# Kernel tuning notes

Measured on AMD Instinct MI355X. Metric: run time of the kernel, lower is better.

## Reference

```python
import jax, jax.numpy as jnp
import numpy as np


def _bd(x, W, b):
    # block-diagonal linear: x [B, D] -> [B, Dout], W [H, D/H, Dout/H], b [Dout]
    B, D = x.shape
    H = W.shape[0]
    y = jnp.einsum('bhi,hio->bho', x.reshape(B, H, D // H), W)
    return y.reshape(B, -1) + b


def setup_inputs() -> dict:
    key = jax.random.key(0)
    ks = jax.random.split(key, 16)
    B, D, H = 8192, 1024, 8
    U = int(D * 4 / 3)  # 1365
    d = D // H          # 128
    s = 0.05
    f32 = jnp.float32
    return {
        'x': jax.random.normal(ks[0], (B, D), f32),
        'h_prev': jax.random.normal(ks[1], (B, D), f32),
        'c_prev': jax.random.normal(ks[2], (B, D), f32),
        'n_prev': jax.random.uniform(ks[3], (B, D), f32) + 0.5,  # positive normalizer state
        'm_prev': jax.random.normal(ks[4], (B, D), f32),
        'ln_g': jnp.ones((D,), f32),
        'ln_b': jnp.zeros((D,), f32),
        'conv_w': jax.random.normal(ks[5], (1, 1, 4), f32) * 0.5,
        'conv_b': jax.random.normal(ks[6], (1,), f32) * 0.1,
        'W': jax.random.normal(ks[7], (4, H, d, d), f32) * s,   # gates z,i,f,o input projections
        'bW': jax.random.normal(ks[8], (4, D), f32) * s,
        'R': jax.random.normal(ks[9], (4, H, d, d), f32) * s,   # gates z,i,f,o recurrent projections
        'bR': jax.random.normal(ks[10], (4, D), f32) * s,
        'upl_w': jax.random.normal(ks[11], (D, U), f32) * s,
        'upl_b': jnp.zeros((U,), f32),
        'upr_w': jax.random.normal(ks[12], (D, U), f32) * s,
        'upr_b': jnp.zeros((U,), f32),
        'down_w': jax.random.normal(ks[13], (U, D), f32) * s,
        'down_b': jnp.zeros((D,), f32),
    }


def reference(x, h_prev, c_prev, n_prev, m_prev, ln_g, ln_b, conv_w, conv_b,
              W, bW, R, bR, upl_w, upl_b, upr_w, upr_b, down_w, down_b):
    # LayerNorm over feature dim (eps matches torch default 1e-5)
    mu = jnp.mean(x, axis=-1, keepdims=True)
    var = jnp.var(x, axis=-1, keepdims=True)
    x_norm = (x - mu) * jax.lax.rsqrt(var + 1e-5) * ln_g + ln_b
    # causal conv1d along the feature axis: kernel 4, left-pad 3 (Conv1d(1,1,4))
    conv = jax.lax.conv_general_dilated(
        x_norm[:, None, :], conv_w, window_strides=(1,), padding=[(3, 0)],
        dimension_numbers=('NCH', 'OIH', 'NCH'))[:, 0, :] + conv_b
    x_conv = jax.nn.silu(conv)
    # block-diagonal gate pre-activations (gate order in W/R stacks: z, i, f, o)
    z = jnp.tanh(_bd(x, W[0], bW[0]) + _bd(h_prev, R[0], bR[0]))
    o = jax.nn.sigmoid(_bd(x, W[3], bW[3]) + _bd(h_prev, R[3], bR[3]))
    i_tilde = _bd(x_conv, W[1], bW[1]) + _bd(h_prev, R[1], bR[1])
    f_tilde = _bd(x_conv, W[2], bW[2]) + _bd(h_prev, R[2], bR[2])
    # stabilized exp-max gating
    m_t = jnp.maximum(f_tilde + m_prev, i_tilde)
    i = jnp.exp(i_tilde - m_t)
    f = jnp.exp(f_tilde + m_prev - m_t)
    c_t = f * c_prev + i * z
    n_t = f * n_prev + i
    h_t = o * c_t / n_t
    # gated MLP (torch F.gelu default = exact erf gelu)
    left = h_t @ upl_w + upl_b
    right = jax.nn.gelu(h_t @ upr_w + upr_b, approximate=False)
    output = (left * right) @ down_w + down_b
    return (output, h_t, c_t, n_t, m_t)
```

## Files before the change

### kernel.cpp

```cpp
#include <hip/hip_runtime.h>
#include <hip/hip_bf16.h>

typedef __attribute__((ext_vector_type(8))) short s8v;
typedef __attribute__((ext_vector_type(4))) float f4v;
typedef unsigned short us4 __attribute__((ext_vector_type(4)));

#define NB 8192
#define ND 1024
#define NH 8
#define NU 1365
#define NUP 1408
#define GK 384
#define GN 512
static const size_t BD = (size_t)NB * ND;

#define WS_AG   ((size_t)0)
#define WS_G    ((size_t)50331648)
#define WS_HBF  ((size_t)73400320)
#define WS_WG   ((size_t)90177536)
#define WS_ULR  ((size_t)93323264)
#define WS_DWNT ((size_t)99090432)

__device__ __forceinline__ void gload16(const void* g, void* l) {
  __builtin_amdgcn_global_load_lds((const __attribute__((address_space(1))) void*)g,
                                   (__attribute__((address_space(3))) void*)l, 16, 0, 0);
}
__device__ __forceinline__ unsigned short tobf(float f) {
  unsigned int u = __float_as_uint(f);
  unsigned int r = (u + 0x7FFFu + ((u >> 16) & 1u)) >> 16;
  return (unsigned short)r;
}
__device__ __forceinline__ float frombf(unsigned short u) {
  return __uint_as_float(((unsigned int)u) << 16);
}
__device__ __forceinline__ float sigm(float x) { return 1.f / (1.f + expf(-x)); }
__device__ __forceinline__ f4v mfma16(s8v a, s8v b, f4v c) {
  return __builtin_amdgcn_mfma_f32_16x16x32_bf16(a, b, c, 0, 0, 0);
}

__global__ __launch_bounds__(256) void prep_kernel(
    const float* __restrict__ W, const float* __restrict__ R,
    const float* __restrict__ upl, const float* __restrict__ upr,
    const float* __restrict__ dwn,
    unsigned short* __restrict__ Wg, unsigned short* __restrict__ ULR,
    unsigned short* __restrict__ Dt) {
  long long idx = (long long)blockIdx.x * 256 + threadIdx.x;
  const long long N1 = (long long)4096 * GK;
  const long long N3 = (long long)2 * NUP * ND;
  const long long N2 = (long long)NUP * ND;
  if (idx < N1) {
    int c = (int)(idx / GK), k = (int)(idx % GK);
    int j = c & 15, g = (c >> 4) & 3, cgrp = (c >> 6) & 7, h = c >> 9;
    int o = cgrp * 16 + j;
    float v = 0.f;
    if (k < 128) {
      if (g == 0 || g == 3) v = W[(((size_t)g * NH + h) * 128 + k) * 128 + o];
    } else if (k < 256) {
      if (g == 1 || g == 2) v = W[(((size_t)g * NH + h) * 128 + (k - 128)) * 128 + o];
    } else {
      v = R[(((size_t)g * NH + h) * 128 + (k - 256)) * 128 + o];
    }
    Wg[idx] = tobf(v);
    return;
  }
  idx -= N1;
  if (idx < N3) {
    int r = (int)(idx / ND), k = (int)(idx % ND);
    int o = (r >> 4) & 1;
    int gcol = (r >> 5) * 16 + (r & 15);
    float v = 0.f;
    if (gcol < NU) v = o ? upr[(size_t)k * NU + gcol] : upl[(size_t)k * NU + gcol];
    ULR[idx] = tobf(v);
    return;
  }
  idx -= N3;
  if (idx < N2) { int n = (int)(idx / NUP), k = (int)(idx % NUP);
    Dt[idx] = (k < NU) ? tobf(dwn[(size_t)k * ND + n]) : 0; return; }
}

__global__ __launch_bounds__(256) void norm_conv(
    const float* __restrict__ x, const float* __restrict__ hp,
    const float* __restrict__ lg, const float* __restrict__ lb,
    const float* __restrict__ cw, const float* __restrict__ cb,
    unsigned short* __restrict__ Ag) {
  const int b = blockIdx.x, tid = threadIdx.x;
  const int lane = tid & 63, wv = tid >> 6;
  __shared__ float xs[1024];
  __shared__ float red[8];
  const int d0 = tid * 4;
  float4 xv = *(const float4*)(x + (size_t)b * ND + d0);
  float s = xv.x + xv.y + xv.z + xv.w;
  float ss = xv.x * xv.x + xv.y * xv.y + xv.z * xv.z + xv.w * xv.w;
#pragma unroll
  for (int o = 32; o; o >>= 1) { s += __shfl_down(s, o); ss += __shfl_down(ss, o); }
  if (lane == 0) { red[wv] = s; red[4 + wv] = ss; }
  __syncthreads();
  float S = red[0] + red[1] + red[2] + red[3];
  float SS = red[4] + red[5] + red[6] + red[7];
  float mu = S * (1.f / ND);
  float var = SS * (1.f / ND) - mu * mu;
  float rstd = rsqrtf(var + 1e-5f);
  float xn[4];
#pragma unroll
  for (int t = 0; t < 4; ++t) {
    float xx = (&xv.x)[t];
    xn[t] = (xx - mu) * rstd * lg[d0 + t] + lb[d0 + t];
    xs[d0 + t] = xn[t];
  }
  __syncthreads();
  float w0 = cw[0], w1 = cw[1], w2 = cw[2], w3 = cw[3], cbv = cb[0];
  float cv[4];
#pragma unroll
  for (int t = 0; t < 4; ++t) {
    int d = d0 + t;
    float a = cbv + w3 * xs[d];
    if (d >= 1) a += w2 * xs[d - 1];
    if (d >= 2) a += w1 * xs[d - 2];
    if (d >= 3) a += w0 * xs[d - 3];
    cv[t] = a * (1.f / (1.f + expf(-a)));
  }
  float4 hv = *(const float4*)(hp + (size_t)b * ND + d0);
  const int h = d0 >> 7, j = d0 & 127;
  us4 px, pc, ph;
#pragma unroll
  for (int t = 0; t < 4; ++t) { px[t] = tobf((&xv.x)[t]); pc[t] = tobf(cv[t]); ph[t] = tobf((&hv.x)[t]); }
  size_t base = (size_t)b * 3072 + (size_t)h * 384 + j;
  *(us4*)(Ag + base) = px;
  *(us4*)(Ag + base + 128) = pc;
  *(us4*)(Ag + base + 256) = ph;
}

__global__ __launch_bounds__(256) void gate_fused(
    const unsigned short* __restrict__ Ag, const unsigned short* __restrict__ Wg,
    const float* __restrict__ bW, const float* __restrict__ bR,
    const float* __restrict__ cp, const float* __restrict__ np_,
    const float* __restrict__ mp,
    float* __restrict__ dout, unsigned short* __restrict__ Hb) {
  __shared__ short As[2][128 * 32];
  __shared__ short Bs[2][128 * 32];
  const int tid = threadIdx.x, lane = tid & 63, wv = tid >> 6;
  const int wm = wv >> 1, wn = wv & 1;
  const int row0 = blockIdx.x * 128;
  const int p = blockIdx.y;
  const int h = blockIdx.z;
  const int srow = wv * 32 + (lane >> 2), scol = (lane & 3) * 8;
  const unsigned short* At = Ag + (size_t)h * 384;
  const unsigned short* Bt = Wg + ((size_t)h * 512 + (size_t)p * 128) * GK;
#define STG(bb, k0)                                                                     \
  do {                                                                                  \
    gload16(At + (size_t)(row0 + srow) * 3072 + (k0) + scol, (char*)As[bb] + wv * 2048);\
    gload16(At + (size_t)(row0 + srow + 16) * 3072 + (k0) + scol,                       \
            (char*)As[bb] + wv * 2048 + 1024);                                          \
    gload16(Bt + (size_t)srow * GK + (k0) + scol, (char*)Bs[bb] + wv * 2048);           \
    gload16(Bt + (size_t)(srow + 16) * GK + (k0) + scol,                                \
            (char*)Bs[bb] + wv * 2048 + 1024);                                          \
  } while (0)
  f4v acc[4][4] = {};
  STG(0, 0);
  __syncthreads();
  for (int kt = 0; kt < 12; ++kt) {
    const int cur = kt & 1;
    if (kt < 11) STG(cur ^ 1, (kt + 1) * 32);
    s8v a[4], b[4];
#pragma unroll
    for (int m = 0; m < 4; ++m)
      a[m] = *(const s8v*)&As[cur][(wm * 64 + m * 16 + (lane & 15)) * 32 + (lane >> 4) * 8];
#pragma unroll
    for (int g = 0; g < 4; ++g)
      b[g] = *(const s8v*)&Bs[cur][(wn * 64 + g * 16 + (lane & 15)) * 32 + (lane >> 4) * 8];
#pragma unroll
    for (int m = 0; m < 4; ++m)
#pragma unroll
      for (int g = 0; g < 4; ++g) acc[m][g] = mfma16(a[m], b[g], acc[m][g]);
    __syncthreads();
  }
#undef STG
  const int cgrp = p * 2 + wn;
  const int gcol = h * 128 + cgrp * 16 + (lane & 15);
  const float Bz = bW[gcol] + bR[gcol];
  const float Bi = bW[ND + gcol] + bR[ND + gcol];
  const float Bf = bW[2 * ND + gcol] + bR[2 * ND + gcol];
  const float Bo = bW[3 * ND + gcol] + bR[3 * ND + gcol];
#pragma unroll
  for (int m = 0; m < 4; ++m) {
    const int rbase = row0 + wm * 64 + m * 16 + (lane >> 4) * 4;
#pragma unroll
    for (int r = 0; r < 4; ++r) {
      const size_t idx = (size_t)(rbase + r) * ND + gcol;
      float zt = tanhf(acc[m][0][r] + Bz);
      float it = acc[m][1][r] + Bi;
      float ft = acc[m][2][r] + Bf;
      float ot = sigm(acc[m][3][r] + Bo);
      float mv = mp[idx];
      float mt = fmaxf(ft + mv, it);
      float ii = expf(it - mt);
      float ff = expf(ft + mv - mt);
      float ct = ff * cp[idx] + ii * zt;
      float nt = ff * np_[idx] + ii;
      float ht = ot * ct / nt;
      dout[BD + idx] = ht;
      dout[2 * BD + idx] = ct;
      dout[3 * BD + idx] = nt;
      dout[4 * BD + idx] = mt;
      Hb[idx] = tobf(ht);
    }
  }
}

__global__ __launch_bounds__(256) void up_gemm(
    const unsigned short* __restrict__ A, const unsigned short* __restrict__ ULR,
    const float* __restrict__ lbias, const float* __restrict__ rbias,
    unsigned short* __restrict__ G) {
  __shared__ short As[2][4096];
  __shared__ short Bs[2][4096];
  const int tid = threadIdx.x, lane = tid & 63, wv = tid >> 6;
  const int wm = wv >> 1, wn = wv & 1;
  const int bid = blockIdx.x;
  const int swz = (bid & 7) * 176 + (bid >> 3);
  const int row0 = (swz / 22) * 128, n0 = (swz % 22) * 128;
  const int srow = wv * 32 + (lane >> 2), scol = (lane & 3) * 8;
#define STG(bb, k0)                                                                       \
  do {                                                                                    \
    gload16(A + (size_t)(row0 + srow) * 1024 + (k0) + scol, (char*)As[bb] + wv * 2048);   \
    gload16(A + (size_t)(row0 + srow + 16) * 1024 + (k0) + scol,                          \
            (char*)As[bb] + wv * 2048 + 1024);                                            \
    gload16(ULR + (size_t)(n0 + srow) * 1024 + (k0) + scol, (char*)Bs[bb] + wv * 2048);   \
    gload16(ULR + (size_t)(n0 + srow + 16) * 1024 + (k0) + scol,                          \
            (char*)Bs[bb] + wv * 2048 + 1024);                                            \
  } while (0)
  f4v acc[4][4] = {};
  STG(0, 0);
  __syncthreads();
  for (int kt = 0; kt < 32; ++kt) {
    const int cur = kt & 1;
    if (kt < 31) STG(cur ^ 1, (kt + 1) * 32);
    s8v a[4], b[4];
#pragma unroll
    for (int m = 0; m < 4; ++m)
      a[m] = *(const s8v*)&As[cur][(wm * 64 + m * 16 + (lane & 15)) * 32 + (lane >> 4) * 8];
#pragma unroll
    for (int n = 0; n < 4; ++n)
      b[n] = *(const s8v*)&Bs[cur][(wn * 64 + n * 16 + (lane & 15)) * 32 + (lane >> 4) * 8];
#pragma unroll
    for (int m = 0; m < 4; ++m)
#pragma unroll
      for (int n = 0; n < 4; ++n) acc[m][n] = mfma16(a[m], b[n], acc[m][n]);
    __syncthreads();
  }
#undef STG
  const int gb = (n0 >> 1) + wn * 32;
#pragma unroll
  for (int m = 0; m < 4; ++m) {
    const int row = row0 + wm * 64 + m * 16 + (lane >> 4) * 4;
#pragma unroll
    for (int p = 0; p < 2; ++p) {
      const int gcol = gb + p * 16 + (lane & 15);
      const bool ok = gcol < NU;
      const float bl_ = ok ? lbias[gcol] : 0.f;
      const float br_ = ok ? rbias[gcol] : 0.f;
#pragma unroll
      for (int r = 0; r < 4; ++r) {
        float L = acc[m][2 * p][r] + bl_;
        float Rv = acc[m][2 * p + 1][r] + br_;
        float ge = 0.5f * Rv * (1.f + erff(Rv * 0.70710678118654752f));
        G[(size_t)(row + r) * NUP + gcol] = ok ? tobf(L * ge) : (unsigned short)0;
      }
    }
  }
}

__global__ __launch_bounds__(256) void down_gemm(
    const unsigned short* __restrict__ A, const unsigned short* __restrict__ Bt,
    const float* __restrict__ dbias, float* __restrict__ out) {
  __shared__ short As[2][4096];
  __shared__ short Bs[2][4096];
  const int tid = threadIdx.x, lane = tid & 63, wv = tid >> 6;
  const int wm = wv >> 1, wn = wv & 1;
  const int bid = blockIdx.x;
  const int swz = (bid & 7) * 64 + (bid >> 3);
  const int row0 = (swz >> 3) * 128, n0 = (swz & 7) * 128;
  const int srow = wv * 32 + (lane >> 2), scol = (lane & 3) * 8;
#define STG(bb, k0)                                                                       \
  do {                                                                                    \
    gload16(A + (size_t)(row0 + srow) * NUP + (k0) + scol, (char*)As[bb] + wv * 2048);    \
    gload16(A + (size_t)(row0 + srow + 16) * NUP + (k0) + scol,                           \
            (char*)As[bb] + wv * 2048 + 1024);                                            \
    gload16(Bt + (size_t)(n0 + srow) * NUP + (k0) + scol, (char*)Bs[bb] + wv * 2048);     \
    gload16(Bt + (size_t)(n0 + srow + 16) * NUP + (k0) + scol,                            \
            (char*)Bs[bb] + wv * 2048 + 1024);                                            \
  } while (0)
  f4v acc[4][4] = {};
  STG(0, 0);
  __syncthreads();
  for (int kt = 0; kt < NUP / 32; ++kt) {
    const int cur = kt & 1;
    if (kt < NUP / 32 - 1) STG(cur ^ 1, (kt + 1) * 32);
    s8v a[4], b[4];
#pragma unroll
    for (int m = 0; m < 4; ++m)
      a[m] = *(const s8v*)&As[cur][(wm * 64 + m * 16 + (lane & 15)) * 32 + (lane >> 4) * 8];
#pragma unroll
    for (int n = 0; n < 4; ++n)
      b[n] = *(const s8v*)&Bs[cur][(wn * 64 + n * 16 + (lane & 15)) * 32 + (lane >> 4) * 8];
#pragma unroll
    for (int m = 0; m < 4; ++m)
#pragma unroll
      for (int n = 0; n < 4; ++n) acc[m][n] = mfma16(a[m], b[n], acc[m][n]);
    __syncthreads();
  }
#undef STG
#pragma unroll
  for (int m = 0; m < 4; ++m) {
    const int row = row0 + wm * 64 + m * 16 + (lane >> 4) * 4;
#pragma unroll
    for (int n = 0; n < 4; ++n) {
      const int col = n0 + wn * 64 + n * 16 + (lane & 15);
      const float bias = dbias[col];
#pragma unroll
      for (int r = 0; r < 4; ++r)
        out[(size_t)(row + r) * ND + col] = acc[m][n][r] + bias;
    }
  }
}

extern "C" void kernel_launch(void* const* d_in, const int* in_sizes, int n_in,
                              void* d_out, int out_size, void* d_ws, size_t ws_size,
                              hipStream_t stream) {
  const float* x    = (const float*)d_in[0];
  const float* hp   = (const float*)d_in[1];
  const float* cp   = (const float*)d_in[2];
  const float* np_  = (const float*)d_in[3];
  const float* mp   = (const float*)d_in[4];
  const float* lg   = (const float*)d_in[5];
  const float* lb   = (const float*)d_in[6];
  const float* cw   = (const float*)d_in[7];
  const float* cb   = (const float*)d_in[8];
  const float* W    = (const float*)d_in[9];
  const float* bW   = (const float*)d_in[10];
  const float* R    = (const float*)d_in[11];
  const float* bR   = (const float*)d_in[12];
  const float* upl  = (const float*)d_in[13];
  const float* uplb = (const float*)d_in[14];
  const float* upr  = (const float*)d_in[15];
  const float* uprb = (const float*)d_in[16];
  const float* dwn  = (const float*)d_in[17];
  const float* dwnb = (const float*)d_in[18];
  float* out = (float*)d_out;
  char* ws = (char*)d_ws;
  unsigned short* Ag  = (unsigned short*)(ws + WS_AG);
  unsigned short* G   = (unsigned short*)(ws + WS_G);
  unsigned short* Hb  = (unsigned short*)(ws + WS_HBF);
  unsigned short* Wg  = (unsigned short*)(ws + WS_WG);
  unsigned short* ULR = (unsigned short*)(ws + WS_ULR);
  unsigned short* Dt  = (unsigned short*)(ws + WS_DWNT);

  prep_kernel<<<23040, 256, 0, stream>>>(W, R, upl, upr, dwn, Wg, ULR, Dt);
  norm_conv<<<NB, 256, 0, stream>>>(x, hp, lg, lb, cw, cb, Ag);
  gate_fused<<<dim3(64, 4, 8), 256, 0, stream>>>(Ag, Wg, bW, bR, cp, np_, mp, out, Hb);
  up_gemm<<<1408, 256, 0, stream>>>(Hb, ULR, uplb, uprb, G);
  down_gemm<<<512, 256, 0, stream>>>(G, Dt, dwnb, out);
}
```

Measured before the change: 276.5 us.

## Drop LDS double buffering; gate GEMM loads fragments directly from global

The gate kernel becomes single-wavefront blocks of 64 rows by 64 gate columns that read MFMA operand fragments straight from global memory, with no LDS staging or barriers and a much larger grid. The up and down GEMMs change from double-buffered LDS staging to single-buffered load, sync, compute, sync loops, which halves LDS use and may raise occupancy. In exchange the GEMMs lose overlap between global loads and MFMA work, and the gate kernel gives up LDS reuse and issues strided uncoalesced global reads that depend on cache hits.

```diff
diff --git a/kernel.cpp b/kernel.cpp
--- a/kernel.cpp
+++ b/kernel.cpp
@@ -130,60 +130,44 @@
   *(us4*)(Ag + base + 256) = ph;
 }
 
-__global__ __launch_bounds__(256) void gate_fused(
+__global__ __launch_bounds__(64, 3) void gate_fused(
     const unsigned short* __restrict__ Ag, const unsigned short* __restrict__ Wg,
     const float* __restrict__ bW, const float* __restrict__ bR,
     const float* __restrict__ cp, const float* __restrict__ np_,
     const float* __restrict__ mp,
     float* __restrict__ dout, unsigned short* __restrict__ Hb) {
-  __shared__ short As[2][128 * 32];
-  __shared__ short Bs[2][128 * 32];
-  const int tid = threadIdx.x, lane = tid & 63, wv = tid >> 6;
-  const int wm = wv >> 1, wn = wv & 1;
-  const int row0 = blockIdx.x * 128;
-  const int p = blockIdx.y;
-  const int h = blockIdx.z;
-  const int srow = wv * 32 + (lane >> 2), scol = (lane & 3) * 8;
-  const unsigned short* At = Ag + (size_t)h * 384;
-  const unsigned short* Bt = Wg + ((size_t)h * 512 + (size_t)p * 128) * GK;
-#define STG(bb, k0)                                                                     \
-  do {                                                                                  \
-    gload16(At + (size_t)(row0 + srow) * 3072 + (k0) + scol, (char*)As[bb] + wv * 2048);\
-    gload16(At + (size_t)(row0 + srow + 16) * 3072 + (k0) + scol,                       \
-            (char*)As[bb] + wv * 2048 + 1024);                                          \
-    gload16(Bt + (size_t)srow * GK + (k0) + scol, (char*)Bs[bb] + wv * 2048);           \
-    gload16(Bt + (size_t)(srow + 16) * GK + (k0) + scol,                                \
-            (char*)Bs[bb] + wv * 2048 + 1024);                                          \
-  } while (0)
+  const int lane = threadIdx.x;
+  const int row0 = blockIdx.x * 64;
+  const int cg = blockIdx.y;
+  const int h = cg >> 3;
+  const unsigned short* Arow =
+      Ag + (size_t)(row0 + (lane & 15)) * 3072 + h * 384 + (lane >> 4) * 8;
+  const unsigned short* Brow =
+      Wg + (size_t)(cg * 64 + (lane & 15)) * GK + (lane >> 4) * 8;
   f4v acc[4][4] = {};
-  STG(0, 0);
-  __syncthreads();
+#pragma unroll
   for (int kt = 0; kt < 12; ++kt) {
-    const int cur = kt & 1;
-    if (kt < 11) STG(cur ^ 1, (kt + 1) * 32);
+    const int k0 = kt * 32;
     s8v a[4], b[4];
 #pragma unroll
     for (int m = 0; m < 4; ++m)
-      a[m] = *(const s8v*)&As[cur][(wm * 64 + m * 16 + (lane & 15)) * 32 + (lane >> 4) * 8];
+      a[m] = *(const s8v*)(Arow + (size_t)m * 16 * 3072 + k0);
 #pragma unroll
     for (int g = 0; g < 4; ++g)
-      b[g] = *(const s8v*)&Bs[cur][(wn * 64 + g * 16 + (lane & 15)) * 32 + (lane >> 4) * 8];
+      b[g] = *(const s8v*)(Brow + (size_t)g * 16 * GK + k0);
 #pragma unroll
     for (int m = 0; m < 4; ++m)
 #pragma unroll
       for (int g = 0; g < 4; ++g) acc[m][g] = mfma16(a[m], b[g], acc[m][g]);
-    __syncthreads();
-  }
-#undef STG
-  const int cgrp = p * 2 + wn;
-  const int gcol = h * 128 + cgrp * 16 + (lane & 15);
+  }
+  const int gcol = h * 128 + (cg & 7) * 16 + (lane & 15);
   const float Bz = bW[gcol] + bR[gcol];
   const float Bi = bW[ND + gcol] + bR[ND + gcol];
   const float Bf = bW[2 * ND + gcol] + bR[2 * ND + gcol];
   const float Bo = bW[3 * ND + gcol] + bR[3 * ND + gcol];
 #pragma unroll
   for (int m = 0; m < 4; ++m) {
-    const int rbase = row0 + wm * 64 + m * 16 + (lane >> 4) * 4;
+    const int rbase = row0 + m * 16 + (lane >> 4) * 4;
 #pragma unroll
     for (int r = 0; r < 4; ++r) {
       const size_t idx = (size_t)(rbase + r) * ND + gcol;
@@ -211,43 +195,33 @@
     const unsigned short* __restrict__ A, const unsigned short* __restrict__ ULR,
     const float* __restrict__ lbias, const float* __restrict__ rbias,
     unsigned short* __restrict__ G) {
-  __shared__ short As[2][4096];
-  __shared__ short Bs[2][4096];
+  __shared__ short As[4096];
+  __shared__ short Bs[4096];
   const int tid = threadIdx.x, lane = tid & 63, wv = tid >> 6;
   const int wm = wv >> 1, wn = wv & 1;
   const int bid = blockIdx.x;
   const int swz = (bid & 7) * 176 + (bid >> 3);
   const int row0 = (swz / 22) * 128, n0 = (swz % 22) * 128;
   const int srow = wv * 32 + (lane >> 2), scol = (lane & 3) * 8;
-#define STG(bb, k0)                                                                       \
-  do {                                                                                    \
-    gload16(A + (size_t)(row0 + srow) * 1024 + (k0) + scol, (char*)As[bb] + wv * 2048);   \
-    gload16(A + (size_t)(row0 + srow + 16) * 1024 + (k0) + scol,                          \
-            (char*)As[bb] + wv * 2048 + 1024);                                            \
-    gload16(ULR + (size_t)(n0 + srow) * 1024 + (k0) + scol, (char*)Bs[bb] + wv * 2048);   \
-    gload16(ULR + (size_t)(n0 + srow + 16) * 1024 + (k0) + scol,                          \
-            (char*)Bs[bb] + wv * 2048 + 1024);                                            \
-  } while (0)
   f4v acc[4][4] = {};
-  STG(0, 0);
-  __syncthreads();
   for (int kt = 0; kt < 32; ++kt) {
-    const int cur = kt & 1;
-    if (kt < 31) STG(cur ^ 1, (kt + 1) * 32);
+    const int k0 = kt * 32;
+    gload16(A + (size_t)(row0 + srow) * 1024 + k0 + scol, (char*)As + wv * 2048);
+    gload16(A + (size_t)(row0 + srow + 16) * 1024 + k0 + scol, (char*)As + wv * 2048 + 1024);
+    gload16(ULR + (size_t)(n0 + srow) * 1024 + k0 + scol, (char*)Bs + wv * 2048);
+    gload16(ULR + (size_t)(n0 + srow + 16) * 1024 + k0 + scol, (char*)Bs + wv * 2048 + 1024);
+    __syncthreads();
     s8v a[4], b[4];
 #pragma unroll
-    for (int m = 0; m < 4; ++m)
-      a[m] = *(const s8v*)&As[cur][(wm * 64 + m * 16 + (lane & 15)) * 32 + (lane >> 4) * 8];
-#pragma unroll
-    for (int n = 0; n < 4; ++n)
-      b[n] = *(const s8v*)&Bs[cur][(wn * 64 + n * 16 + (lane & 15)) * 32 + (lane >> 4) * 8];
+    for (int m = 0; m < 4; ++m) a[m] = *(const s8v*)&As[(wm * 64 + m * 16 + (lane & 15)) * 32 + (lane >> 4) * 8];
+#pragma unroll
+    for (int n = 0; n < 4; ++n) b[n] = *(const s8v*)&Bs[(wn * 64 + n * 16 + (lane & 15)) * 32 + (lane >> 4) * 8];
 #pragma unroll
     for (int m = 0; m < 4; ++m)
 #pragma unroll
       for (int n = 0; n < 4; ++n) acc[m][n] = mfma16(a[m], b[n], acc[m][n]);
     __syncthreads();
   }
-#undef STG
   const int gb = (n0 >> 1) + wn * 32;
 #pragma unroll
   for (int m = 0; m < 4; ++m) {
@@ -272,43 +246,33 @@
 __global__ __launch_bounds__(256) void down_gemm(
     const unsigned short* __restrict__ A, const unsigned short* __restrict__ Bt,
     const float* __restrict__ dbias, float* __restrict__ out) {
-  __shared__ short As[2][4096];
-  __shared__ short Bs[2][4096];
+  __shared__ short As[4096];
+  __shared__ short Bs[4096];
   const int tid = threadIdx.x, lane = tid & 63, wv = tid >> 6;
   const int wm = wv >> 1, wn = wv & 1;
   const int bid = blockIdx.x;
   const int swz = (bid & 7) * 64 + (bid >> 3);
   const int row0 = (swz >> 3) * 128, n0 = (swz & 7) * 128;
   const int srow = wv * 32 + (lane >> 2), scol = (lane & 3) * 8;
-#define STG(bb, k0)                                                                       \
-  do {                                                                                    \
-    gload16(A + (size_t)(row0 + srow) * NUP + (k0) + scol, (char*)As[bb] + wv * 2048);    \
-    gload16(A + (size_t)(row0 + srow + 16) * NUP + (k0) + scol,                           \
-            (char*)As[bb] + wv * 2048 + 1024);                                            \
-    gload16(Bt + (size_t)(n0 + srow) * NUP + (k0) + scol, (char*)Bs[bb] + wv * 2048);     \
-    gload16(Bt + (size_t)(n0 + srow + 16) * NUP + (k0) + scol,                            \
-            (char*)Bs[bb] + wv * 2048 + 1024);                                            \
-  } while (0)
   f4v acc[4][4] = {};
-  STG(0, 0);
-  __syncthreads();
   for (int kt = 0; kt < NUP / 32; ++kt) {
-    const int cur = kt & 1;
-    if (kt < NUP / 32 - 1) STG(cur ^ 1, (kt + 1) * 32);
+    const int k0 = kt * 32;
+    gload16(A + (size_t)(row0 + srow) * NUP + k0 + scol, (char*)As + wv * 2048);
+    gload16(A + (size_t)(row0 + srow + 16) * NUP + k0 + scol, (char*)As + wv * 2048 + 1024);
+    gload16(Bt + (size_t)(n0 + srow) * NUP + k0 + scol, (char*)Bs + wv * 2048);
+    gload16(Bt + (size_t)(n0 + srow + 16) * NUP + k0 + scol, (char*)Bs + wv * 2048 + 1024);
+    __syncthreads();
     s8v a[4], b[4];
 #pragma unroll
-    for (int m = 0; m < 4; ++m)
-      a[m] = *(const s8v*)&As[cur][(wm * 64 + m * 16 + (lane & 15)) * 32 + (lane >> 4) * 8];
-#pragma unroll
-    for (int n = 0; n < 4; ++n)
-      b[n] = *(const s8v*)&Bs[cur][(wn * 64 + n * 16 + (lane & 15)) * 32 + (lane >> 4) * 8];
+    for (int m = 0; m < 4; ++m) a[m] = *(const s8v*)&As[(wm * 64 + m * 16 + (lane & 15)) * 32 + (lane >> 4) * 8];
+#pragma unroll
+    for (int n = 0; n < 4; ++n) b[n] = *(const s8v*)&Bs[(wn * 64 + n * 16 + (lane & 15)) * 32 + (lane >> 4) * 8];
 #pragma unroll
     for (int m = 0; m < 4; ++m)
 #pragma unroll
       for (int n = 0; n < 4; ++n) acc[m][n] = mfma16(a[m], b[n], acc[m][n]);
     __syncthreads();
   }
-#undef STG
 #pragma unroll
   for (int m = 0; m < 4; ++m) {
     const int row = row0 + wm * 64 + m * 16 + (lane >> 4) * 4;
@@ -356,7 +320,7 @@
 
   prep_kernel<<<23040, 256, 0, stream>>>(W, R, upl, upr, dwn, Wg, ULR, Dt);
   norm_conv<<<NB, 256, 0, stream>>>(x, hp, lg, lb, cw, cb, Ag);
-  gate_fused<<<dim3(64, 4, 8), 256, 0, stream>>>(Ag, Wg, bW, bR, cp, np_, mp, out, Hb);
+  gate_fused<<<dim3(128, 64), 64, 0, stream>>>(Ag, Wg, bW, bR, cp, np_, mp, out, Hb);
   up_gemm<<<1408, 256, 0, stream>>>(Hb, ULR, uplb, uprb, G);
   down_gemm<<<512, 256, 0, stream>>>(G, Dt, dwnb, out);
 }
```

New measurement: 332.7 us. +20.3%, slower.
